# Optimization experiments

Measured on AMD Instinct MI355X. Metric: run time of the kernel, lower is better.

## Reference

```python
import jax, jax.numpy as jnp
import numpy as np

WINDOW = 128
CAUSAL = True
LOOK_BACKWARD = 1
LOOK_FORWARD = 0  # causal forces look_forward = 0


def _look_around(x, backward, forward, pad_value, dim):
    # pad along window axis (axis=1), then concat shifted slices along `dim`
    nw = x.shape[1]
    pad_cfg = [(0, 0)] * x.ndim
    pad_cfg[1] = (backward, forward)
    padded = jnp.pad(x, pad_cfg, constant_values=pad_value)
    slices = [padded[:, i:i + nw] for i in range(forward + backward + 1)]
    return jnp.concatenate(slices, axis=dim)


def setup_inputs() -> dict:
    key = jax.random.key(0)
    kq, kk, kv = jax.random.split(key, 3)
    shape = (2, 16, 4096, 64)
    return {
        "q": jax.random.normal(kq, shape, dtype=jnp.float32),
        "k": jax.random.normal(kk, shape, dtype=jnp.float32),
        "v": jax.random.normal(kv, shape, dtype=jnp.float32),
    }


def reference(q, k, v):
    b, h, t, e = q.shape
    scale = e ** (-0.5)
    windows = t // WINDOW  # t assumed divisible by WINDOW (pad_to_multiple is no-op)

    # merge batch and heads, bucket into windows
    bq = q.reshape(b * h, windows, WINDOW, e)
    bk = k.reshape(b * h, windows, WINDOW, e)
    bv = v.reshape(b * h, windows, WINDOW, e)

    # look-around gather of key/value windows: j-dim = WINDOW*(1+back+fwd)
    bk = _look_around(bk, LOOK_BACKWARD, LOOK_FORWARD, 0.0, dim=2)
    bv = _look_around(bv, LOOK_BACKWARD, LOOK_FORWARD, 0.0, dim=2)

    # positional indices for masking
    bq_t = jnp.arange(t).reshape(1, windows, WINDOW)
    bq_k = _look_around(bq_t, LOOK_BACKWARD, LOOK_FORWARD, -1, dim=2)

    mask = (bq_k == -1)[:, :, None, :]  # (1, w, 1, j) padded positions
    if CAUSAL:
        mask = mask | (bq_t[:, :, :, None] < bq_k[:, :, None, :])

    dots = jnp.einsum('bwie,bwje->bwij', bq * scale, bk)
    mask_value = -jnp.finfo(dots.dtype).max
    dots = jnp.where(mask, mask_value, dots)
    attn = jax.nn.softmax(dots.astype(jnp.float32), axis=-1).astype(dots.dtype)
    out = jnp.einsum('bwij,bwje->bwie', attn, bv)
    return out.reshape(b, h, t, e)
```

## Files before the change

### kernel.cpp

```cpp
#include <hip/hip_runtime.h>

#define T_DIM 4096
#define E_DIM 64
#define WIN   128
#define NWIN  (T_DIM / WIN)
#define KS_LD 72
#define VT_LD 136
#define OS_LD 68

typedef __bf16  bf16x4 __attribute__((ext_vector_type(4)));
typedef __bf16  bf16x8 __attribute__((ext_vector_type(8)));
typedef float   f32x16 __attribute__((ext_vector_type(16)));

__global__ __launch_bounds__(256, 3)
void la_fwd(const float* __restrict__ Q, const float* __restrict__ K,
            const float* __restrict__ V, float* __restrict__ O)
{
  __shared__ __align__(16) unsigned char lds_raw[53248];
  __bf16* Ks  = (__bf16*)(lds_raw);
  __bf16* Vt0 = (__bf16*)(lds_raw + 18432);
  __bf16* Vt1 = (__bf16*)(lds_raw + 35840);
  float*  Os  = (float*)(lds_raw);

  const int tid  = threadIdx.x;
  const int lane = tid & 63;
  const int wid  = tid >> 6;
  const int col  = lane & 31;
  const int half = lane >> 5;

  const int w  = blockIdx.x;
  const int bh = blockIdx.y;

  const float* Qb = Q + (size_t)bh * T_DIM * E_DIM;
  const float* Kb = K + (size_t)bh * T_DIM * E_DIM;
  const float* Vb = V + (size_t)bh * T_DIM * E_DIM;
  float*       Ob = O + (size_t)bh * T_DIM * E_DIM;

  const int q0 = w * WIN;
  const int e0 = (tid & 15) << 2;
  const int jb = (tid >> 4) << 2;

  const float* kp1 = Kb + (size_t)q0 * E_DIM;
  const float* vp1 = Vb + (size_t)q0 * E_DIM;
  const float* kp0 = kp1 - WIN * E_DIM;
  const float* vp0 = vp1 - WIN * E_DIM;

  float4 k0f[8], v0f[8], k1f[8], v1f[8], qf[8];
  if (w > 0) {
#pragma unroll
    for (int i = 0; i < 8; ++i) k0f[i] = *(const float4*)(kp0 + (i << 10) + (tid << 2));
#pragma unroll
    for (int p = 0; p < 2; ++p)
#pragma unroll
      for (int r = 0; r < 4; ++r)
        v0f[p * 4 + r] = *(const float4*)(vp0 + (size_t)(p * 64 + jb + r) * E_DIM + e0);
  }
#pragma unroll
  for (int i = 0; i < 8; ++i) k1f[i] = *(const float4*)(kp1 + (i << 10) + (tid << 2));
#pragma unroll
  for (int p = 0; p < 2; ++p)
#pragma unroll
    for (int r = 0; r < 4; ++r)
      v1f[p * 4 + r] = *(const float4*)(vp1 + (size_t)(p * 64 + jb + r) * E_DIM + e0);
  {
    const float* qrow = Qb + (size_t)(q0 + wid * 32 + col) * E_DIM;
#pragma unroll
    for (int c = 0; c < 4; ++c) {
      qf[2 * c]     = *(const float4*)(qrow + c * 16 + half * 8);
      qf[2 * c + 1] = *(const float4*)(qrow + c * 16 + half * 8 + 4);
    }
  }

  auto cvt8 = [&](const float4* src, bf16x4* dst) {
#pragma unroll
    for (int i = 0; i < 8; ++i) {
      const float* f = (const float*)&src[i];
      bf16x4 b;
      b[0] = (__bf16)f[0]; b[1] = (__bf16)f[1]; b[2] = (__bf16)f[2]; b[3] = (__bf16)f[3];
      dst[i] = b;
    }
  };
  bf16x4 k0b[8], v0b[8], k1b[8], v1b[8];
  if (w > 0) { cvt8(k0f, k0b); cvt8(v0f, v0b); }
  cvt8(k1f, k1b); cvt8(v1f, v1b);

  const float QS = 0.125f * 1.44269504088896340736f;
  bf16x8 bq[4];
#pragma unroll
  for (int c = 0; c < 4; ++c) {
    const float* x = (const float*)&qf[2 * c];
    const float* y = (const float*)&qf[2 * c + 1];
    bf16x8 a;
    a[0]=(__bf16)(x[0]*QS); a[1]=(__bf16)(x[1]*QS); a[2]=(__bf16)(x[2]*QS); a[3]=(__bf16)(x[3]*QS);
    a[4]=(__bf16)(y[0]*QS); a[5]=(__bf16)(y[1]*QS); a[6]=(__bf16)(y[2]*QS); a[7]=(__bf16)(y[3]*QS);
    bq[c] = a;
  }

  auto writeK = [&](const bf16x4* ksrc) {
#pragma unroll
    for (int i = 0; i < 8; ++i) {
      const int fi = (i << 10) + (tid << 2);
      *(bf16x4*)(&Ks[(fi >> 6) * KS_LD + (fi & 63)]) = ksrc[i];
    }
  };
  auto writeV = [&](const bf16x4* vsrc, __bf16* Vt) {
#pragma unroll
    for (int p = 0; p < 2; ++p)
#pragma unroll
      for (int c = 0; c < 4; ++c) {
        bf16x4 t;
        t[0] = vsrc[p*4+0][c]; t[1] = vsrc[p*4+1][c];
        t[2] = vsrc[p*4+2][c]; t[3] = vsrc[p*4+3][c];
        *(bf16x4*)(&Vt[(e0 + c) * VT_LD + p * 64 + jb]) = t;
      }
  };

  if (w > 0) { writeK(k0b); writeV(v0b, Vt0); }
  else       { writeK(k1b); }
  writeV(v1b, Vt1);

  float  lsum = 0.0f;
  f32x16 oacc[2];
#pragma unroll
  for (int et = 0; et < 2; ++et)
#pragma unroll
    for (int r = 0; r < 16; ++r) oacc[et][r] = 0.0f;

  __syncthreads();

  auto kb_step = [&](const __bf16* Vt, int kb, bool diag) {
    f32x16 s;
#pragma unroll
    for (int r = 0; r < 16; ++r) s[r] = 0.0f;
#pragma unroll
    for (int c = 0; c < 4; ++c) {
      const bf16x8 a = *(const bf16x8*)(&Ks[(kb * 32 + col) * KS_LD + c * 16 + half * 8]);
      s = __builtin_amdgcn_mfma_f32_32x32x16_bf16(a, bq[c], s, 0, 0, 0);
    }
    float pr[16];
#pragma unroll
    for (int r = 0; r < 16; ++r) {
      const int key = (r & 3) + 8 * (r >> 2) + 4 * half;
      float sv = s[r];
      if (diag && key > col) sv = -3.0e38f;
      const float p = __builtin_amdgcn_exp2f(sv);
      lsum += p;
      pr[r] = p;
    }
#pragma unroll
    for (int g = 0; g < 2; ++g) {
      int A0, A1, B0, B1;
      asm("v_cvt_pk_bf16_f32 %0, %1, %2" : "=v"(A0) : "v"(pr[8*g+0]), "v"(pr[8*g+1]));
      asm("v_cvt_pk_bf16_f32 %0, %1, %2" : "=v"(A1) : "v"(pr[8*g+2]), "v"(pr[8*g+3]));
      asm("v_cvt_pk_bf16_f32 %0, %1, %2" : "=v"(B0) : "v"(pr[8*g+4]), "v"(pr[8*g+5]));
      asm("v_cvt_pk_bf16_f32 %0, %1, %2" : "=v"(B1) : "v"(pr[8*g+6]), "v"(pr[8*g+7]));
      asm("v_permlane32_swap_b32 %0, %1" : "+v"(A0), "+v"(B0));
      asm("v_permlane32_swap_b32 %0, %1" : "+v"(A1), "+v"(B1));
      union { int d[4]; bf16x8 v; } u;
      u.d[0] = A0; u.d[1] = A1; u.d[2] = B0; u.d[3] = B1;
      const int j0 = kb * 32 + g * 16 + half * 8;
#pragma unroll
      for (int et = 0; et < 2; ++et) {
        const bf16x8 bv = *(const bf16x8*)(&Vt[(et * 32 + col) * VT_LD + j0]);
        oacc[et] = __builtin_amdgcn_mfma_f32_32x32x16_bf16(u.v, bv, oacc[et], 0, 0, 0);
      }
    }
  };

  if (w > 0) {
#pragma unroll
    for (int kb = 0; kb < 4; ++kb) kb_step(Vt0, kb, false);
    __syncthreads();
    writeK(k1b);
    __syncthreads();
  }
#pragma unroll
  for (int kb = 0; kb < 4; ++kb)
    if (kb <= wid) kb_step(Vt1, kb, kb == wid);

  float xx = lsum, yy = lsum;
  asm("v_permlane32_swap_b32 %0, %1" : "+v"(xx), "+v"(yy));
  const float ltot = xx + yy;

  __syncthreads();
#pragma unroll
  for (int r = 0; r < 16; ++r) {
    const int row = (r & 3) + 8 * (r >> 2) + 4 * half;
    const float lq   = __int_as_float(__builtin_amdgcn_ds_bpermute(row << 2, __float_as_int(ltot)));
    const float rinv = __builtin_amdgcn_rcpf(lq);
    Os[(wid * 32 + row) * OS_LD + col]      = oacc[0][r] * rinv;
    Os[(wid * 32 + row) * OS_LD + col + 32] = oacc[1][r] * rinv;
  }
  __syncthreads();
  {
    float* ob = Ob + (size_t)q0 * E_DIM;
#pragma unroll
    for (int i = 0; i < 8; ++i) {
      const int fi = (i << 10) + (tid << 2);
      const float4 o4 = *(const float4*)(&Os[(fi >> 6) * OS_LD + (fi & 63)]);
      *(float4*)(ob + fi) = o4;
    }
  }
}

extern "C" void kernel_launch(void* const* d_in, const int* in_sizes, int n_in,
                              void* d_out, int out_size, void* d_ws, size_t ws_size,
                              hipStream_t stream) {
  const float* Q = (const float*)d_in[0];
  const float* K = (const float*)d_in[1];
  const float* V = (const float*)d_in[2];
  float*       O = (float*)d_out;
  const int bh = in_sizes[0] / (T_DIM * E_DIM);
  dim3 grid(NWIN, bh);
  la_fwd<<<grid, 256, 0, stream>>>(Q, K, V, O);
}
```

Baseline: 136.5 us.

## Share one swizzled V buffer to cut LDS and raise occupancy, remap block grid

Replaces the two transposed V buffers with a single XOR-swizzled buffer that is rewritten between the previous and current window phases. This shrinks shared memory from 52KB to 35KB so launch bounds can request four blocks per CU instead of three, and the swizzle is meant to reduce LDS bank conflicts on the V reads. The grid is flattened and remapped so neighbouring blocks come from different heads, which spreads work across XCDs, and the Q loads are issued before the current-window K/V loads. In exchange it adds an extra V transpose write inside the synchronised section and hardcodes the flat-index mapping for 32 heads and 32 windows.

After: 168.5 us. 23.4% more time.

```diff
diff --git a/kernel.cpp b/kernel.cpp
--- a/kernel.cpp
+++ b/kernel.cpp
@@ -5,21 +5,20 @@
 #define WIN   128
 #define NWIN  (T_DIM / WIN)
 #define KS_LD 72
-#define VT_LD 136
+#define VT_ROW 272
 #define OS_LD 68
 
 typedef __bf16  bf16x4 __attribute__((ext_vector_type(4)));
 typedef __bf16  bf16x8 __attribute__((ext_vector_type(8)));
 typedef float   f32x16 __attribute__((ext_vector_type(16)));
 
-__global__ __launch_bounds__(256, 3)
+__global__ __launch_bounds__(256, 4)
 void la_fwd(const float* __restrict__ Q, const float* __restrict__ K,
             const float* __restrict__ V, float* __restrict__ O)
 {
-  __shared__ __align__(16) unsigned char lds_raw[53248];
+  __shared__ __align__(16) unsigned char lds_raw[35840];
   __bf16* Ks  = (__bf16*)(lds_raw);
-  __bf16* Vt0 = (__bf16*)(lds_raw + 18432);
-  __bf16* Vt1 = (__bf16*)(lds_raw + 35840);
+  char*   Vtb = (char*)(lds_raw + 18432);
   float*  Os  = (float*)(lds_raw);
 
   const int tid  = threadIdx.x;
@@ -28,8 +27,9 @@
   const int col  = lane & 31;
   const int half = lane >> 5;
 
-  const int w  = blockIdx.x;
-  const int bh = blockIdx.y;
+  const int flat = blockIdx.x;
+  const int w  = (flat >> 3) & 31;
+  const int bh = (flat & 7) * 4 + (flat >> 8);
 
   const float* Qb = Q + (size_t)bh * T_DIM * E_DIM;
   const float* Kb = K + (size_t)bh * T_DIM * E_DIM;
@@ -55,13 +55,6 @@
       for (int r = 0; r < 4; ++r)
         v0f[p * 4 + r] = *(const float4*)(vp0 + (size_t)(p * 64 + jb + r) * E_DIM + e0);
   }
-#pragma unroll
-  for (int i = 0; i < 8; ++i) k1f[i] = *(const float4*)(kp1 + (i << 10) + (tid << 2));
-#pragma unroll
-  for (int p = 0; p < 2; ++p)
-#pragma unroll
-    for (int r = 0; r < 4; ++r)
-      v1f[p * 4 + r] = *(const float4*)(vp1 + (size_t)(p * 64 + jb + r) * E_DIM + e0);
   {
     const float* qrow = Qb + (size_t)(q0 + wid * 32 + col) * E_DIM;
 #pragma unroll
@@ -70,6 +63,13 @@
       qf[2 * c + 1] = *(const float4*)(qrow + c * 16 + half * 8 + 4);
     }
   }
+#pragma unroll
+  for (int i = 0; i < 8; ++i) k1f[i] = *(const float4*)(kp1 + (i << 10) + (tid << 2));
+#pragma unroll
+  for (int p = 0; p < 2; ++p)
+#pragma unroll
+    for (int r = 0; r < 4; ++r)
+      v1f[p * 4 + r] = *(const float4*)(vp1 + (size_t)(p * 64 + jb + r) * E_DIM + e0);
 
   auto cvt8 = [&](const float4* src, bf16x4* dst) {
 #pragma unroll
@@ -103,7 +103,7 @@
       *(bf16x4*)(&Ks[(fi >> 6) * KS_LD + (fi & 63)]) = ksrc[i];
     }
   };
-  auto writeV = [&](const bf16x4* vsrc, __bf16* Vt) {
+  auto writeV = [&](const bf16x4* vsrc) {
 #pragma unroll
     for (int p = 0; p < 2; ++p)
 #pragma unroll
@@ -111,13 +111,14 @@
         bf16x4 t;
         t[0] = vsrc[p*4+0][c]; t[1] = vsrc[p*4+1][c];
         t[2] = vsrc[p*4+2][c]; t[3] = vsrc[p*4+3][c];
-        *(bf16x4*)(&Vt[(e0 + c) * VT_LD + p * 64 + jb]) = t;
+        const int e = e0 + c;
+        const int boff = (2 * (p * 64 + jb)) ^ (((e >> 3) & 1) << 5);
+        *(bf16x4*)(Vtb + e * VT_ROW + boff) = t;
       }
   };
 
-  if (w > 0) { writeK(k0b); writeV(v0b, Vt0); }
-  else       { writeK(k1b); }
-  writeV(v1b, Vt1);
+  if (w > 0) { writeK(k0b); writeV(v0b); }
+  else       { writeK(k1b); writeV(v1b); }
 
   float  lsum = 0.0f;
   f32x16 oacc[2];
@@ -128,7 +129,7 @@
 
   __syncthreads();
 
-  auto kb_step = [&](const __bf16* Vt, int kb, bool diag) {
+  auto kb_step = [&](int kb, bool diag) {
     f32x16 s;
 #pragma unroll
     for (int r = 0; r < 16; ++r) s[r] = 0.0f;
@@ -158,10 +159,10 @@
       asm("v_permlane32_swap_b32 %0, %1" : "+v"(A1), "+v"(B1));
       union { int d[4]; bf16x8 v; } u;
       u.d[0] = A0; u.d[1] = A1; u.d[2] = B0; u.d[3] = B1;
-      const int j0 = kb * 32 + g * 16 + half * 8;
+      const int j0b = (kb * 64 + g * 32 + half * 16) ^ (((col >> 3) & 1) << 5);
 #pragma unroll
       for (int et = 0; et < 2; ++et) {
-        const bf16x8 bv = *(const bf16x8*)(&Vt[(et * 32 + col) * VT_LD + j0]);
+        const bf16x8 bv = *(const bf16x8*)(Vtb + (et * 32 + col) * VT_ROW + j0b);
         oacc[et] = __builtin_amdgcn_mfma_f32_32x32x16_bf16(u.v, bv, oacc[et], 0, 0, 0);
       }
     }
@@ -169,14 +170,14 @@
 
   if (w > 0) {
 #pragma unroll
-    for (int kb = 0; kb < 4; ++kb) kb_step(Vt0, kb, false);
+    for (int kb = 0; kb < 4; ++kb) kb_step(kb, false);
     __syncthreads();
-    writeK(k1b);
+    writeK(k1b); writeV(v1b);
     __syncthreads();
   }
 #pragma unroll
   for (int kb = 0; kb < 4; ++kb)
-    if (kb <= wid) kb_step(Vt1, kb, kb == wid);
+    if (kb <= wid) kb_step(kb, kb == wid);
 
   float xx = lsum, yy = lsum;
   asm("v_permlane32_swap_b32 %0, %1" : "+v"(xx), "+v"(yy));
@@ -211,6 +212,5 @@
   const float* V = (const float*)d_in[2];
   float*       O = (float*)d_out;
   const int bh = in_sizes[0] / (T_DIM * E_DIM);
-  dim3 grid(NWIN, bh);
-  la_fwd<<<grid, 256, 0, stream>>>(Q, K, V, O);
+  la_fwd<<<dim3(NWIN * bh), 256, 0, stream>>>(Q, K, V, O);
 }
```
